# Kernel tuning notes

Hardware: AMD Instinct MI355X
Metric: run time of the kernel (lower is better)

## Reference

```python
import math
import jax, jax.numpy as jnp
import numpy as np

D_MODEL = 1024
MAX_LEN = 5000
N_DIAS = 512
DIA_LEN = 64
TOTAL = N_DIAS * DIA_LEN  # 32768 tokens


def make_pe(max_len: int, d_model: int) -> jnp.ndarray:
    # Matches torch: pe[:, 0::2] = sin(pos*div), pe[:, 1::2] = cos(pos*div)
    position = jnp.arange(max_len, dtype=jnp.float32)[:, None]           # [L,1]
    div_term = jnp.exp(jnp.arange(0, d_model, 2, dtype=jnp.float32)
                       * (-math.log(10000.0) / d_model))                 # [d/2]
    pe = jnp.zeros((max_len, d_model), dtype=jnp.float32)
    pe = pe.at[:, 0::2].set(jnp.sin(position * div_term))
    pe = pe.at[:, 1::2].set(jnp.cos(position * div_term))
    return pe


def setup_inputs() -> dict:
    key = jax.random.key(0)
    x = jax.random.normal(key, (TOTAL, D_MODEL), dtype=jnp.float32)
    dia_len = jnp.full((N_DIAS,), DIA_LEN, dtype=jnp.int64 if jax.config.jax_enable_x64 else jnp.int32)
    pe = make_pe(MAX_LEN, D_MODEL)
    return {"x": x, "pe": pe, "dia_len": dia_len}


def reference(x, pe, dia_len):
    # Original loop: for each dialogue of length i, out[tmp:tmp+i] = x[tmp:tmp+i] + pe[:i]
    # i.e. positions restart at 0 for every dialogue segment.
    N = x.shape[0]
    offsets = jnp.cumsum(dia_len) - dia_len                 # start offset of each segment
    seg_start = jnp.repeat(offsets, dia_len, total_repeat_length=N)  # [N]
    pos = jnp.arange(N, dtype=seg_start.dtype) - seg_start  # position within segment
    out = x + pe[pos]                                       # fused gather-add
    # Dropout is identity in eval mode (reference baseline).
    return out
```

## Files before the change

kernel.cpp:

```cpp
#include <hip/hip_runtime.h>

__global__ void __launch_bounds__(512)
pe_fused_kernel(const float4* __restrict__ x,
                const float4* __restrict__ pe,
                const int* __restrict__ dia_len, int n_seg,
                float4* __restrict__ out, long n4) {
    __shared__ int cum[512];
    const int t = threadIdx.x;
    int v = (t < n_seg) ? dia_len[t] : 0;
    cum[t] = v;
    __syncthreads();
    #pragma unroll
    for (int off = 1; off < 512; off <<= 1) {
        int add = (t >= off) ? cum[t - off] : 0;
        __syncthreads();
        cum[t] += add;
        __syncthreads();
    }

    long i = (long)blockIdx.x * blockDim.x + threadIdx.x;
    const long stride = (long)gridDim.x * blockDim.x;
    for (; i < n4; i += stride) {
        const int row = (int)(i >> 8);
        int lo = 0, hi = n_seg;
        while (lo < hi) {
            const int mid = (lo + hi) >> 1;
            if (cum[mid] > row) hi = mid; else lo = mid + 1;
        }
        const int start = (lo > 0) ? cum[lo - 1] : 0;
        const int p = row - start;
        const float4 xv = x[i];
        const float4 pv = pe[((long)p << 8) | (i & 255)];
        float4 o;
        o.x = xv.x + pv.x;
        o.y = xv.y + pv.y;
        o.z = xv.z + pv.z;
        o.w = xv.w + pv.w;
        out[i] = o;
    }
}

extern "C" void kernel_launch(void* const* d_in, const int* in_sizes, int n_in,
                              void* d_out, int out_size, void* d_ws, size_t ws_size,
                              hipStream_t stream) {
    const float* x  = (const float*)d_in[0];
    const float* pe = (const float*)d_in[1];
    const int*   dl = (const int*)d_in[2];
    float*       out = (float*)d_out;

    const int n_seg = in_sizes[2];
    const long n4 = (long)out_size / 4;

    pe_fused_kernel<<<1024, 512, 0, stream>>>(
        (const float4*)x, (const float4*)pe, dl, n_seg, (float4*)out, n4);
}
```

Before: 50.44 us.

## Replace per-element binary search with bucketed segment lookup table and unroll by two

Builds an exclusive prefix-sum array plus a shared-memory bucket table that maps each 64-row block to its first segment. Each element then finds its segment with a table lookup and a short linear scan instead of a nine-step binary search in LDS. The grid-stride loop is also unrolled by two so more loads are in flight. The bucket table holds only 512 entries, indexed by row>>6, so it covers at most 32768 rows and would overflow for longer totals. Setup also gains extra barriers and a per-segment fill loop in every block.

Measured after the change: 50.80 us. No clear change (+0.7%).

```diff
diff --git a/kernel.cpp b/kernel.cpp
--- a/kernel.cpp
+++ b/kernel.cpp
@@ -5,39 +5,51 @@
                 const float4* __restrict__ pe,
                 const int* __restrict__ dia_len, int n_seg,
                 float4* __restrict__ out, long n4) {
-    __shared__ int cum[512];
+    __shared__ int ex[513];
+    __shared__ int seg_lo[512];
     const int t = threadIdx.x;
-    int v = (t < n_seg) ? dia_len[t] : 0;
-    cum[t] = v;
+
+    seg_lo[t] = (t < n_seg) ? dia_len[t] : 0;
     __syncthreads();
     #pragma unroll
     for (int off = 1; off < 512; off <<= 1) {
-        int add = (t >= off) ? cum[t - off] : 0;
+        int add = (t >= off) ? seg_lo[t - off] : 0;
         __syncthreads();
-        cum[t] += add;
+        seg_lo[t] += add;
         __syncthreads();
     }
+    ex[t + 1] = seg_lo[t];
+    if (t == 0) ex[0] = 0;
+    __syncthreads();
+    if (t < n_seg) {
+        const int st = ex[t], en = ex[t + 1];
+        for (int b = (st + 63) >> 6; (b << 6) < en; ++b) seg_lo[b] = t;
+    }
+    __syncthreads();
 
+    const long stride = (long)gridDim.x * blockDim.x;
     long i = (long)blockIdx.x * blockDim.x + threadIdx.x;
-    const long stride = (long)gridDim.x * blockDim.x;
-    for (; i < n4; i += stride) {
-        const int row = (int)(i >> 8);
-        int lo = 0, hi = n_seg;
-        while (lo < hi) {
-            const int mid = (lo + hi) >> 1;
-            if (cum[mid] > row) hi = mid; else lo = mid + 1;
+
+    #define PE_BODY(I)                                                \
+        {                                                             \
+            const int row = (int)((I) >> 8);                          \
+            int s = seg_lo[row >> 6];                                 \
+            while (ex[s + 1] <= row) ++s;   \
+            const int p = row - ex[s];                                \
+            const float4 xv = x[(I)];                                 \
+            const float4 pv = pe[((long)p << 8) | ((I) & 255)];       \
+            float4 o;                                                 \
+            o.x = xv.x + pv.x; o.y = xv.y + pv.y;                     \
+            o.z = xv.z + pv.z; o.w = xv.w + pv.w;                     \
+            out[(I)] = o;                                             \
         }
-        const int start = (lo > 0) ? cum[lo - 1] : 0;
-        const int p = row - start;
-        const float4 xv = x[i];
-        const float4 pv = pe[((long)p << 8) | (i & 255)];
-        float4 o;
-        o.x = xv.x + pv.x;
-        o.y = xv.y + pv.y;
-        o.z = xv.z + pv.z;
-        o.w = xv.w + pv.w;
-        out[i] = o;
+
+    for (; i + stride < n4; i += 2 * stride) {
+        PE_BODY(i);
+        PE_BODY(i + stride);
     }
+    for (; i < n4; i += stride) PE_BODY(i);
+    #undef PE_BODY
 }
 
 extern "C" void kernel_launch(void* const* d_in, const int* in_sizes, int n_in,
```

## Precompute per-row positions in a separate kernel and simplify streaming add

Applied to the files above, without the earlier changes.

Splits the work into two kernels. The first computes, per segment, its start offset with a wave reduction and writes a per-row position table into workspace. The second does the gather-add using that table with an 8-way unrolled, one-pass grid and nontemporal stores. This removes the per-block 512-element prefix scan and the per-element binary search, but adds a second launch and a workspace round trip.

New measurement: 49.58 us. Within noise of the previous version (-1.7%).

```diff
diff --git a/kernel.cpp b/kernel.cpp
--- a/kernel.cpp
+++ b/kernel.cpp
@@ -1,42 +1,38 @@
 #include <hip/hip_runtime.h>
 
-__global__ void __launch_bounds__(512)
-pe_fused_kernel(const float4* __restrict__ x,
-                const float4* __restrict__ pe,
-                const int* __restrict__ dia_len, int n_seg,
-                float4* __restrict__ out, long n4) {
-    __shared__ int cum[512];
+typedef float f4 __attribute__((ext_vector_type(4)));
+
+__global__ void __launch_bounds__(64)
+pe_pos_kernel(const int* __restrict__ dia_len, int n_seg,
+              int* __restrict__ pos) {
+    const int b = blockIdx.x;
     const int t = threadIdx.x;
-    int v = (t < n_seg) ? dia_len[t] : 0;
-    cum[t] = v;
-    __syncthreads();
+    int partial = 0;
+    for (int j = t; j < b; j += 64) partial += dia_len[j];
     #pragma unroll
-    for (int off = 1; off < 512; off <<= 1) {
-        int add = (t >= off) ? cum[t - off] : 0;
-        __syncthreads();
-        cum[t] += add;
-        __syncthreads();
-    }
+    for (int off = 32; off > 0; off >>= 1)
+        partial += __shfl_down(partial, off, 64);
+    const int start = __shfl(partial, 0, 64);
+    const int len = dia_len[b];
+    for (int k = t; k < len; k += 64) pos[start + k] = k;
+}
 
-    long i = (long)blockIdx.x * blockDim.x + threadIdx.x;
-    const long stride = (long)gridDim.x * blockDim.x;
-    for (; i < n4; i += stride) {
-        const int row = (int)(i >> 8);
-        int lo = 0, hi = n_seg;
-        while (lo < hi) {
-            const int mid = (lo + hi) >> 1;
-            if (cum[mid] > row) hi = mid; else lo = mid + 1;
+__global__ void __launch_bounds__(256)
+pe_add_kernel(const f4* __restrict__ x,
+              const f4* __restrict__ pe,
+              const int* __restrict__ pos,
+              f4* __restrict__ out, long n4) {
+    const long base = (long)blockIdx.x * 2048 + threadIdx.x;
+    #pragma unroll
+    for (int u = 0; u < 8; ++u) {
+        const long i = base + (long)u * 256;
+        if (i < n4) {
+            const int row = (int)(i >> 8);
+            const int p = pos[row];
+            const f4 a = x[i];
+            const f4 b = pe[((long)p << 8) | (i & 255)];
+            __builtin_nontemporal_store(a + b, &out[i]);
         }
-        const int start = (lo > 0) ? cum[lo - 1] : 0;
-        const int p = row - start;
-        const float4 xv = x[i];
-        const float4 pv = pe[((long)p << 8) | (i & 255)];
-        float4 o;
-        o.x = xv.x + pv.x;
-        o.y = xv.y + pv.y;
-        o.z = xv.z + pv.z;
-        o.w = xv.w + pv.w;
-        out[i] = o;
     }
 }
 
@@ -46,11 +42,14 @@
     const float* x  = (const float*)d_in[0];
     const float* pe = (const float*)d_in[1];
     const int*   dl = (const int*)d_in[2];
-    float*       out = (float*)d_out;
 
     const int n_seg = in_sizes[2];
     const long n4 = (long)out_size / 4;
+    int* pos = (int*)d_ws;
 
-    pe_fused_kernel<<<1024, 512, 0, stream>>>(
-        (const float4*)x, (const float4*)pe, dl, n_seg, (float4*)out, n4);
+    pe_pos_kernel<<<n_seg, 64, 0, stream>>>(dl, n_seg, pos);
+
+    const int nblk = (int)((n4 + 2047) / 2048);
+    pe_add_kernel<<<nblk, 256, 0, stream>>>(
+        (const f4*)x, (const f4*)pe, pos, (f4*)d_out, n4);
 }
```
